# Optimization experiments

Hardware: AMD Instinct MI355X
Metric: run time of the kernel (lower is better)

## Reference

```python
import jax, jax.numpy as jnp
import numpy as np

EPS = 1e-5


def _conv(x, w, groups=1):
    # x: NCHW, w: OIHW, stride 1, padding k//2 == SAME for k=3
    return jax.lax.conv_general_dilated(
        x, w, window_strides=(1, 1), padding='SAME',
        feature_group_count=groups,
        dimension_numbers=('NCHW', 'OIHW', 'NCHW'))


def _bn(x, gamma, beta, mean, var):
    # eval-mode BatchNorm2d
    s = gamma * jax.lax.rsqrt(var + EPS)
    return x * s[None, :, None, None] + (beta - mean * s)[None, :, None, None]


def _bilinear_up_kernel(ch, k):
    # dla_up.fill_up_weights: bilinear upsampling kernel, shape (ch, 1, k, k)
    f = (k + 1) // 2
    c = (2 * f - 1 - f % 2) / (2.0 * f)
    i = np.arange(k)
    w1d = 1.0 - np.abs(i / f - c)
    w2d = np.outer(w1d, w1d).astype(np.float32)  # (k, k)
    return jnp.asarray(np.broadcast_to(w2d, (ch, 1, k, k)).copy())


def setup_inputs() -> dict:
    key = jax.random.key(0)
    ks = jax.random.split(key, 8)
    B, C, H, W = 16, 32, 128, 128
    OUT, NL = 8, 4
    layers = jax.random.normal(ks[0], (NL + 1, B, C, H, W), jnp.float32)
    node_w = jax.random.normal(ks[1], (NL, C, 2 * C, 3, 3), jnp.float32) * 0.05
    node_gamma = jnp.ones((NL, C), jnp.float32)
    node_beta = jnp.zeros((NL, C), jnp.float32)
    node_mean = jax.random.normal(ks[2], (NL, C), jnp.float32) * 0.1
    node_var = jax.random.uniform(ks[3], (NL, C), jnp.float32, 0.5, 1.5)
    final_w = jax.random.normal(ks[4], (OUT, C, 3, 3), jnp.float32) * 0.05
    final_gamma = jnp.ones((OUT,), jnp.float32)
    final_beta = jnp.zeros((OUT,), jnp.float32)
    final_mean = jax.random.normal(ks[5], (OUT,), jnp.float32) * 0.1
    final_var = jax.random.uniform(ks[6], (OUT,), jnp.float32, 0.5, 1.5)
    up_w = _bilinear_up_kernel(OUT, 4)  # frozen depthwise transpose-conv weight
    return dict(layers=layers, node_w=node_w, node_gamma=node_gamma,
                node_beta=node_beta, node_mean=node_mean, node_var=node_var,
                final_w=final_w, final_gamma=final_gamma, final_beta=final_beta,
                final_mean=final_mean, final_var=final_var, up_w=up_w)


def reference(layers, node_w, node_gamma, node_beta, node_mean, node_var,
              final_w, final_gamma, final_beta, final_mean, final_var, up_w):
    x = layers[0]
    n_layers = node_w.shape[0]
    for i in range(n_layers):  # fixed small structural loop
        h = jnp.concatenate([x, layers[i + 1]], axis=1)  # [B, 2C, H, W]
        x = jax.nn.relu(_bn(_conv(h, node_w[i]),
                            node_gamma[i], node_beta[i], node_mean[i], node_var[i]))
    x = jnp.tanh(_bn(_conv(x, final_w),
                     final_gamma, final_beta, final_mean, final_var))
    # depthwise ConvTranspose2d(k=4, stride=2, pad=1): equivalent fractionally
    # strided conv with flipped kernel, lhs_dilation=2, padding k-1-pad=2
    groups = up_w.shape[0]
    x = jax.lax.conv_general_dilated(
        x, up_w[:, :, ::-1, ::-1], window_strides=(1, 1),
        padding=[(2, 2), (2, 2)], lhs_dilation=(2, 2),
        feature_group_count=groups,
        dimension_numbers=('NCHW', 'OIHW', 'NCHW'))  # [B, OUT, 2H, 2W]
    # vectorized form of the per-row / per-col delta loops
    Ho, Wo = x.shape[2], x.shape[3]
    row_ramp = jnp.arange(Ho, dtype=x.dtype) / Ho  # delta_i = i / H
    col_ramp = jnp.arange(Wo, dtype=x.dtype) / Wo  # delta_j = j / W
    x = x.at[:, 0].add(row_ramp[None, :, None])
    x = x.at[:, 1].add(col_ramp[None, None, :])
    return x
```

## Files before the change

### kernel.cpp

```cpp
#include <hip/hip_runtime.h>
#include <hip/hip_bf16.h>
#include <cmath>

using bf16 = __hip_bfloat16;
typedef _Float16 f16x8 __attribute__((ext_vector_type(8)));
typedef float f32x16 __attribute__((ext_vector_type(16)));

__device__ __forceinline__ float ldin(const void* p, size_t i, int f) {
    return f ? ((const float*)p)[i] : __bfloat162float(((const bf16*)p)[i]);
}

__device__ __forceinline__ float bfu(unsigned short u) {
    union { unsigned u32; float f; } x; x.u32 = (unsigned)u << 16; return x.f;
}

__device__ __forceinline__ int swq(int X) { return (X + (X >> 2)) & 3; }

__global__ void detect_kernel(const unsigned short* __restrict__ u, int* __restrict__ flag) {
    __shared__ int s_bad;
    if (threadIdx.x == 0) s_bad = 0;
    __syncthreads();
    int base = blockIdx.x * 256 + threadIdx.x;
    int bad = 0;
#pragma unroll
    for (int k = 0; k < 4; ++k) {
        unsigned short v = u[2 * (base + k * 16384)];
        int e = (v >> 7) & 0xFF;
        if (e == 0xFF || (e == 0 && (v & 0x7FFF))) bad++;
    }
    if (bad) atomicAdd(&s_bad, bad);
    __syncthreads();
    if (threadIdx.x == 0 && s_bad) atomicAdd(&flag[1], s_bad);
}

__global__ void pack_kernel(const void* __restrict__ nw, const void* __restrict__ ng,
                            const void* __restrict__ nb, const void* __restrict__ nm,
                            const void* __restrict__ nv, const void* __restrict__ fw,
                            const void* __restrict__ fg, const void* __restrict__ fb,
                            const void* __restrict__ fm, const void* __restrict__ fv,
                            const void* __restrict__ upw, const int* __restrict__ flag,
                            char* __restrict__ ws) {
    const int f = flag[1] > 32;
    int i = blockIdx.x * 256 + threadIdx.x;
    _Float16* wpkN = (_Float16*)(ws + 160);
    _Float16* wpkF = (_Float16*)(ws + 147616);
    float* upwf  = (float*)(ws + 166048);
    float* nbias = (float*)(ws + 166560);
    float* fbias = (float*)(ws + 167072);
    if (i < 73728) {
        int e = i & 7, lane = (i >> 3) & 63, rest = i >> 9;
        int t = rest % 9, rest2 = rest / 9;
        int kc = rest2 & 3, lay = rest2 >> 2;
        int oc = lane & 31, ic = kc * 16 + ((lane >> 5) << 3) + e;
        float s = ldin(ng, lay * 32 + oc, f) * rsqrtf(ldin(nv, lay * 32 + oc, f) + 1e-5f);
        float w = ldin(nw, ((size_t)(lay * 32 + oc) * 64 + ic) * 9 + t, f);
        wpkN[i] = (_Float16)(w * s);
    } else if (i < 82944) {
        int j = i - 73728;
        int e = j & 7, lane = (j >> 3) & 63, rest = j >> 9;
        int t = rest % 9, kc = rest / 9;
        int oc = lane & 31, ic = kc * 16 + ((lane >> 5) << 3) + e;
        float v = 0.f;
        if (oc < 8) {
            float s = ldin(fg, oc, f) * rsqrtf(ldin(fv, oc, f) + 1e-5f);
            v = ldin(fw, ((size_t)(oc * 32 + ic)) * 9 + t, f) * s;
        }
        wpkF[j] = (_Float16)v;
    } else if (i < 83072) {
        int k = i - 82944;
        upwf[k] = ldin(upw, k, f);
    } else if (i < 83200) {
        int k = i - 83072;
        float s = ldin(ng, k, f) * rsqrtf(ldin(nv, k, f) + 1e-5f);
        nbias[k] = ldin(nb, k, f) - ldin(nm, k, f) * s;
    } else if (i < 83232) {
        int k = i - 83200;
        float v = 0.f;
        if (k < 8) {
            float s = ldin(fg, k, f) * rsqrtf(ldin(fv, k, f) + 1e-5f);
            v = ldin(fb, k, f) - ldin(fm, k, f) * s;
        }
        fbias[k] = v;
    }
}

__device__ __forceinline__ void stage_nchw_g(char* lds, const void* src,
                                             size_t base_elem, int f, int tid,
                                             int x0g, int y0g) {
    for (int job = tid; job < 1360; job += 256) {
        int c = job / 340, rest = job - c * 340;
        int row = rest / 34, X = rest - row * 34;
        int gy = y0g - 1 + row, gx = x0g - 1 + X;
        union { _Float16 h[8]; uint4 v; } pk;
        if (gy >= 0 && gy < 128 && gx >= 0 && gx < 128) {
            size_t e0 = base_elem + (size_t)(c * 8) * 16384 + (size_t)gy * 128 + gx;
            if (f) {
#pragma unroll
                for (int j = 0; j < 8; ++j)
                    pk.h[j] = (_Float16)(((const float*)src)[e0 + (size_t)j * 16384]);
            } else {
#pragma unroll
                for (int j = 0; j < 8; ++j)
                    pk.h[j] = (_Float16)bfu(((const unsigned short*)src)[e0 + (size_t)j * 16384]);
            }
        } else {
            pk.v = make_uint4(0u, 0u, 0u, 0u);
        }
        int slot = (c + swq(X)) & 3;
        *(uint4*)(lds + row * 2176 + (X << 6) + (slot << 4)) = pk.v;
    }
}

__device__ __forceinline__ void stage_nhwc(char* lds, const _Float16* xh, int tid,
                                           int b, int x0g, int y0g) {
    for (int q = tid; q < 1360; q += 256) {
        int p = q >> 2, s = q & 3;
        int row = p / 34, X = p - row * 34;
        int c = (s - swq(X)) & 3;
        int gy = y0g - 1 + row, gx = x0g - 1 + X;
        uint4 v = {0u, 0u, 0u, 0u};
        if (gy >= 0 && gy < 128 && gx >= 0 && gx < 128)
            v = *(const uint4*)(xh + (((size_t)(b * 128 + gy) * 128 + gx) * 32 + c * 8));
        *(uint4*)(lds + (q << 4)) = v;
    }
}

__device__ __forceinline__ void conv_plane(const char* lds, const _Float16* wseg,
                                           int lane, int wid, int lh,
                                           f32x16& acc0, f32x16& acc1) {
    const int l31 = lane & 31;
#pragma unroll
    for (int kc = 0; kc < 2; ++kc) {
        f16x8 bfr[9];
#pragma unroll
        for (int t = 0; t < 9; ++t)
            bfr[t] = *(const f16x8*)(wseg + (size_t)((kc * 9 + t) * 64 + lane) * 8);
        const int chunk = (kc << 1) | lh;
#pragma unroll
        for (int iy = 0; iy < 4; ++iy) {
            const int rowoff = ((wid << 1) + iy) * 2176;
#pragma unroll
            for (int kx = 0; kx < 3; ++kx) {
                const int X = l31 + kx;
                const int slot = (chunk + swq(X)) & 3;
                const f16x8 a = *(const f16x8*)(lds + rowoff + (X << 6) + (slot << 4));
#pragma unroll
                for (int ky = 0; ky < 3; ++ky) {
                    const int y = iy - ky;
                    if (y == 0)
                        acc0 = __builtin_amdgcn_mfma_f32_32x32x16_f16(a, bfr[ky * 3 + kx], acc0, 0, 0, 0);
                    else if (y == 1)
                        acc1 = __builtin_amdgcn_mfma_f32_32x32x16_f16(a, bfr[ky * 3 + kx], acc1, 0, 0, 0);
                }
            }
        }
    }
}

__global__ __launch_bounds__(256, 3) void node_conv_mfma(
    const void* __restrict__ xprev, int xprev_nchw, int xprev_slice,
    const void* __restrict__ layers, int skip_slice,
    const _Float16* __restrict__ wl, const float* __restrict__ bias,
    const int* __restrict__ flag, _Float16* __restrict__ out) {
    __shared__ char lds[21760];
    const int f = flag[1] > 32;
    const int tid = threadIdx.x;
    const int x0g = blockIdx.x << 5, y0g = blockIdx.y << 3, b = blockIdx.z;
    const int lane = tid & 63, wid = tid >> 6;
    const int l31 = lane & 31, lh = lane >> 5;

    f32x16 acc0, acc1;
#pragma unroll
    for (int r = 0; r < 16; ++r) { acc0[r] = 0.f; acc1[r] = 0.f; }

    if (xprev_nchw)
        stage_nchw_g(lds, xprev, (size_t)xprev_slice * 8388608 + (size_t)b * 524288,
                     f, tid, x0g, y0g);
    else
        stage_nhwc(lds, (const _Float16*)xprev, tid, b, x0g, y0g);
    __syncthreads();
    conv_plane(lds, wl, lane, wid, lh, acc0, acc1);
    __syncthreads();

    stage_nchw_g(lds, layers, (size_t)skip_slice * 8388608 + (size_t)b * 524288,
                 f, tid, x0g, y0g);
    __syncthreads();
    conv_plane(lds, wl + 9216, lane, wid, lh, acc0, acc1);

    const float bs = bias[l31];
    {
        const int gy = y0g + (wid << 1);
#pragma unroll
        for (int r = 0; r < 16; ++r) {
            const int xr = (r & 3) + ((r >> 2) << 3) + (lh << 2);
            out[((size_t)(b * 128 + gy) * 128 + (x0g + xr)) * 32 + l31] =
                (_Float16)fmaxf(acc0[r] + bs, 0.f);
        }
#pragma unroll
        for (int r = 0; r < 16; ++r) {
            const int xr = (r & 3) + ((r >> 2) << 3) + (lh << 2);
            out[((size_t)(b * 128 + gy + 1) * 128 + (x0g + xr)) * 32 + l31] =
                (_Float16)fmaxf(acc1[r] + bs, 0.f);
        }
    }
}

__device__ __forceinline__ float ftanh(float x) {
    float e = __expf(2.f * x);
    return 1.f - 2.f / (e + 1.f);
}

__global__ __launch_bounds__(256, 3) void final_conv_mfma(
    const _Float16* __restrict__ xin, const _Float16* __restrict__ wf,
    const float* __restrict__ fbias, _Float16* __restrict__ outF) {
    __shared__ char lds[21760];
    const int tid = threadIdx.x;
    const int x0g = blockIdx.x << 5, y0g = blockIdx.y << 3, b = blockIdx.z;
    const int lane = tid & 63, wid = tid >> 6;
    const int l31 = lane & 31, lh = lane >> 5;

    stage_nhwc(lds, xin, tid, b, x0g, y0g);
    __syncthreads();

    f32x16 acc0, acc1;
#pragma unroll
    for (int r = 0; r < 16; ++r) { acc0[r] = 0.f; acc1[r] = 0.f; }
    conv_plane(lds, wf, lane, wid, lh, acc0, acc1);

    const float bs = fbias[l31];
    if (l31 < 8) {
        const int gy = y0g + (wid << 1);
#pragma unroll
        for (int r = 0; r < 16; ++r) {
            const int xr = (r & 3) + ((r >> 2) << 3) + (lh << 2);
            outF[((size_t)(b * 128 + gy) * 128 + (x0g + xr)) * 8 + l31] =
                (_Float16)ftanh(acc0[r] + bs);
        }
#pragma unroll
        for (int r = 0; r < 16; ++r) {
            const int xr = (r & 3) + ((r >> 2) << 3) + (lh << 2);
            outF[((size_t)(b * 128 + gy + 1) * 128 + (x0g + xr)) * 8 + l31] =
                (_Float16)ftanh(acc1[r] + bs);
        }
    }
}

__global__ __launch_bounds__(256) void upsample_q(
    const _Float16* __restrict__ F, const float* __restrict__ wf,
    const int* __restrict__ flag, void* __restrict__ out) {
    const int f = flag[1] > 32;
    int i = blockIdx.x * 256 + threadIdx.x;
    int qx = i & 127, qy = (i >> 7) & 127, b = i >> 14;

    f16x8 inb[3][3];
#pragma unroll
    for (int jy = 0; jy < 3; ++jy)
#pragma unroll
        for (int jx = 0; jx < 3; ++jx) {
            int iy = qy - 1 + jy, ix = qx - 1 + jx;
            f16x8 v;
#pragma unroll
            for (int c = 0; c < 8; ++c) v[c] = (_Float16)0.f;
            if (iy >= 0 && iy < 128 && ix >= 0 && ix < 128)
                v = *(const f16x8*)(F + (((size_t)(b * 128 + iy) * 128 + ix) << 3));
            inb[jy][jx] = v;
        }

    float acc[32];
#pragma unroll
    for (int k = 0; k < 32; ++k) acc[k] = 0.f;
#pragma unroll
    for (int ky = 0; ky < 4; ++ky) {
        const int dy = 1 - (ky & 1), jy = 2 - ((ky + 1) >> 1);
#pragma unroll
        for (int kx = 0; kx < 4; ++kx) {
            const int dx = 1 - (kx & 1), jx = 2 - ((kx + 1) >> 1);
            const f16x8 p = inb[jy][jx];
#pragma unroll
            for (int c = 0; c < 8; ++c)
                acc[c * 4 + dy * 2 + dx] =
                    fmaf((float)p[c], wf[c * 16 + ky * 4 + kx], acc[c * 4 + dy * 2 + dx]);
        }
    }
#pragma unroll
    for (int d = 0; d < 4; ++d) {
        acc[d]     += (float)(2 * qy + (d >> 1)) * (1.0f / 256.0f);
        acc[4 + d] += (float)(2 * qx + (d & 1)) * (1.0f / 256.0f);
    }
#pragma unroll
    for (int c = 0; c < 8; ++c)
#pragma unroll
        for (int dy2 = 0; dy2 < 2; ++dy2) {
            size_t a = ((size_t)(b * 8 + c) * 256 + (qy * 2 + dy2)) * 256 + qx * 2;
            float v0 = acc[c * 4 + dy2 * 2], v1 = acc[c * 4 + dy2 * 2 + 1];
            if (f) {
                *(float2*)((float*)out + a) = make_float2(v0, v1);
            } else {
                union { bf16 h; unsigned short u; } u0, u1;
                u0.h = __float2bfloat16(v0); u1.h = __float2bfloat16(v1);
                ((unsigned*)out)[a >> 1] = (unsigned)u0.u | ((unsigned)u1.u << 16);
            }
        }
}

extern "C" void kernel_launch(void* const* d_in, const int* in_sizes, int n_in,
                              void* d_out, int out_size, void* d_ws, size_t ws_size,
                              hipStream_t stream) {
    const void* layers = d_in[0];
    const void* node_w = d_in[1];
    const void* ng     = d_in[2];
    const void* nb     = d_in[3];
    const void* nm     = d_in[4];
    const void* nv     = d_in[5];
    const void* fw     = d_in[6];
    const void* fg     = d_in[7];
    const void* fb     = d_in[8];
    const void* fm     = d_in[9];
    const void* fv     = d_in[10];
    const void* upw    = d_in[11];

    char* ws = (char*)d_ws;
    int* dflag       = (int*)d_ws;
    _Float16* wpkN   = (_Float16*)(ws + 160);
    _Float16* wpkF   = (_Float16*)(ws + 147616);
    float* upwf      = (float*)(ws + 166048);
    float* nbias     = (float*)(ws + 166560);
    float* fbias     = (float*)(ws + 167072);
    _Float16* X      = (_Float16*)(ws + 167424);
    _Float16* Y      = (_Float16*)d_out;

    hipMemsetAsync(dflag, 0, 16, stream);
    detect_kernel<<<64, 256, 0, stream>>>((const unsigned short*)layers, dflag);
    pack_kernel<<<326, 256, 0, stream>>>(node_w, ng, nb, nm, nv,
                                         fw, fg, fb, fm, fv, upw, dflag, ws);

    dim3 g(4, 16, 16), blk(256);
    node_conv_mfma<<<g, blk, 0, stream>>>(layers, 1, 0, layers, 1,
                                          wpkN, nbias, dflag, X);
    node_conv_mfma<<<g, blk, 0, stream>>>(X, 0, 0, layers, 2,
                                          wpkN + 18432, nbias + 32, dflag, Y);
    node_conv_mfma<<<g, blk, 0, stream>>>(Y, 0, 0, layers, 3,
                                          wpkN + 2 * 18432, nbias + 64, dflag, X);
    node_conv_mfma<<<g, blk, 0, stream>>>(X, 0, 0, layers, 4,
                                          wpkN + 3 * 18432, nbias + 96, dflag, Y);
    final_conv_mfma<<<g, blk, 0, stream>>>(Y, wpkF, fbias, X);
    upsample_q<<<1024, 256, 0, stream>>>(X, upwf, dflag, d_out);
}
```

Before: 482.0 us.

## Stage both conv inputs at once, coalesce outputs via LDS, fold dtype detect into pack

The node conv now stages the previous activation and the skip layer into two LDS halves before a single barrier and runs all four K-chunks in one pass, which removes the mid-kernel barrier and staging serialization. Both node and final conv outputs are transposed through LDS and written as 16-byte coalesced stores instead of scattered 2-byte stores. The separate memset and detect kernels are dropped; each pack block does its own bf16/fp32 sampling detection and writes the flag to the workspace. Staging loops are fully unrolled. Doubling LDS per block may reduce occupancy below the requested three blocks per CU.

Result: faster. 388.8 us (-19.3%).

```diff
diff --git a/kernel.cpp b/kernel.cpp
--- a/kernel.cpp
+++ b/kernel.cpp
@@ -16,21 +16,21 @@
 
 __device__ __forceinline__ int swq(int X) { return (X + (X >> 2)) & 3; }
 
-__global__ void detect_kernel(const unsigned short* __restrict__ u, int* __restrict__ flag) {
+__device__ __forceinline__ int detect_f(const void* layers_) {
+    const unsigned short* u = (const unsigned short*)layers_;
     __shared__ int s_bad;
     if (threadIdx.x == 0) s_bad = 0;
     __syncthreads();
-    int base = blockIdx.x * 256 + threadIdx.x;
     int bad = 0;
 #pragma unroll
-    for (int k = 0; k < 4; ++k) {
-        unsigned short v = u[2 * (base + k * 16384)];
+    for (int k = 0; k < 16; ++k) {
+        unsigned short v = u[2 * ((threadIdx.x * 16 + k) * 257)];
         int e = (v >> 7) & 0xFF;
-        if (e == 0xFF || (e == 0 && (v & 0x7FFF))) bad++;
+        bad += (e == 0xFF || (e == 0 && (v & 0x7FFF))) ? 1 : 0;
     }
     if (bad) atomicAdd(&s_bad, bad);
     __syncthreads();
-    if (threadIdx.x == 0 && s_bad) atomicAdd(&flag[1], s_bad);
+    return s_bad > 0;
 }
 
 __global__ void pack_kernel(const void* __restrict__ nw, const void* __restrict__ ng,
@@ -38,9 +38,10 @@
                             const void* __restrict__ nv, const void* __restrict__ fw,
                             const void* __restrict__ fg, const void* __restrict__ fb,
                             const void* __restrict__ fm, const void* __restrict__ fv,
-                            const void* __restrict__ upw, const int* __restrict__ flag,
+                            const void* __restrict__ upw, const void* __restrict__ layers_,
                             char* __restrict__ ws) {
-    const int f = flag[1] > 32;
+    const int f = detect_f(layers_);
+    if (blockIdx.x == 0 && threadIdx.x == 0) *(volatile int*)ws = f;
     int i = blockIdx.x * 256 + threadIdx.x;
     _Float16* wpkN = (_Float16*)(ws + 160);
     _Float16* wpkF = (_Float16*)(ws + 147616);
@@ -87,55 +88,64 @@
 __device__ __forceinline__ void stage_nchw_g(char* lds, const void* src,
                                              size_t base_elem, int f, int tid,
                                              int x0g, int y0g) {
-    for (int job = tid; job < 1360; job += 256) {
-        int c = job / 340, rest = job - c * 340;
-        int row = rest / 34, X = rest - row * 34;
-        int gy = y0g - 1 + row, gx = x0g - 1 + X;
-        union { _Float16 h[8]; uint4 v; } pk;
-        if (gy >= 0 && gy < 128 && gx >= 0 && gx < 128) {
-            size_t e0 = base_elem + (size_t)(c * 8) * 16384 + (size_t)gy * 128 + gx;
-            if (f) {
-#pragma unroll
-                for (int j = 0; j < 8; ++j)
-                    pk.h[j] = (_Float16)(((const float*)src)[e0 + (size_t)j * 16384]);
+#pragma unroll
+    for (int it = 0; it < 6; ++it) {
+        int job = tid + it * 256;
+        if (it < 5 || job < 1360) {
+            int c = job / 340, rest = job - c * 340;
+            int row = rest / 34, X = rest - row * 34;
+            int gy = y0g - 1 + row, gx = x0g - 1 + X;
+            union { _Float16 h[8]; uint4 v; } pk;
+            if (gy >= 0 && gy < 128 && gx >= 0 && gx < 128) {
+                size_t e0 = base_elem + (size_t)(c * 8) * 16384 + (size_t)gy * 128 + gx;
+                if (f) {
+#pragma unroll
+                    for (int j = 0; j < 8; ++j)
+                        pk.h[j] = (_Float16)(((const float*)src)[e0 + (size_t)j * 16384]);
+                } else {
+#pragma unroll
+                    for (int j = 0; j < 8; ++j)
+                        pk.h[j] = (_Float16)bfu(((const unsigned short*)src)[e0 + (size_t)j * 16384]);
+                }
             } else {
-#pragma unroll
-                for (int j = 0; j < 8; ++j)
-                    pk.h[j] = (_Float16)bfu(((const unsigned short*)src)[e0 + (size_t)j * 16384]);
+                pk.v = make_uint4(0u, 0u, 0u, 0u);
             }
-        } else {
-            pk.v = make_uint4(0u, 0u, 0u, 0u);
-        }
-        int slot = (c + swq(X)) & 3;
-        *(uint4*)(lds + row * 2176 + (X << 6) + (slot << 4)) = pk.v;
+            int slot = (c + swq(X)) & 3;
+            *(uint4*)(lds + row * 2176 + (X << 6) + (slot << 4)) = pk.v;
+        }
     }
 }
 
 __device__ __forceinline__ void stage_nhwc(char* lds, const _Float16* xh, int tid,
                                            int b, int x0g, int y0g) {
-    for (int q = tid; q < 1360; q += 256) {
-        int p = q >> 2, s = q & 3;
-        int row = p / 34, X = p - row * 34;
-        int c = (s - swq(X)) & 3;
-        int gy = y0g - 1 + row, gx = x0g - 1 + X;
-        uint4 v = {0u, 0u, 0u, 0u};
-        if (gy >= 0 && gy < 128 && gx >= 0 && gx < 128)
-            v = *(const uint4*)(xh + (((size_t)(b * 128 + gy) * 128 + gx) * 32 + c * 8));
-        *(uint4*)(lds + (q << 4)) = v;
-    }
-}
-
-__device__ __forceinline__ void conv_plane(const char* lds, const _Float16* wseg,
-                                           int lane, int wid, int lh,
-                                           f32x16& acc0, f32x16& acc1) {
+#pragma unroll
+    for (int it = 0; it < 6; ++it) {
+        int q = tid + it * 256;
+        if (it < 5 || q < 1360) {
+            int p = q >> 2, s = q & 3;
+            int row = p / 34, X = p - row * 34;
+            int c = (s - swq(X)) & 3;
+            int gy = y0g - 1 + row, gx = x0g - 1 + X;
+            uint4 v = {0u, 0u, 0u, 0u};
+            if (gy >= 0 && gy < 128 && gx >= 0 && gx < 128)
+                v = *(const uint4*)(xh + (((size_t)(b * 128 + gy) * 128 + gx) * 32 + c * 8));
+            *(uint4*)(lds + (q << 4)) = v;
+        }
+    }
+}
+
+__device__ __forceinline__ void conv_both(const char* lds, const _Float16* wseg,
+                                          int lane, int wid, int lh,
+                                          f32x16& acc0, f32x16& acc1) {
     const int l31 = lane & 31;
 #pragma unroll
-    for (int kc = 0; kc < 2; ++kc) {
+    for (int kc = 0; kc < 4; ++kc) {
         f16x8 bfr[9];
 #pragma unroll
         for (int t = 0; t < 9; ++t)
             bfr[t] = *(const f16x8*)(wseg + (size_t)((kc * 9 + t) * 64 + lane) * 8);
-        const int chunk = (kc << 1) | lh;
+        const char* pl = lds + ((kc & 2) ? 21760 : 0);
+        const int chunk = ((kc & 1) << 1) | lh;
 #pragma unroll
         for (int iy = 0; iy < 4; ++iy) {
             const int rowoff = ((wid << 1) + iy) * 2176;
@@ -143,7 +153,7 @@
             for (int kx = 0; kx < 3; ++kx) {
                 const int X = l31 + kx;
                 const int slot = (chunk + swq(X)) & 3;
-                const f16x8 a = *(const f16x8*)(lds + rowoff + (X << 6) + (slot << 4));
+                const f16x8 a = *(const f16x8*)(pl + rowoff + (X << 6) + (slot << 4));
 #pragma unroll
                 for (int ky = 0; ky < 3; ++ky) {
                     const int y = iy - ky;
@@ -157,51 +167,83 @@
     }
 }
 
+__device__ __forceinline__ void conv_plane(const char* lds, const _Float16* wseg,
+                                           int lane, int wid, int lh,
+                                           f32x16& acc0, f32x16& acc1) {
+    const int l31 = lane & 31;
+#pragma unroll
+    for (int kc = 0; kc < 2; ++kc) {
+        f16x8 bfr[9];
+#pragma unroll
+        for (int t = 0; t < 9; ++t)
+            bfr[t] = *(const f16x8*)(wseg + (size_t)((kc * 9 + t) * 64 + lane) * 8);
+        const int chunk = (kc << 1) | lh;
+#pragma unroll
+        for (int iy = 0; iy < 4; ++iy) {
+            const int rowoff = ((wid << 1) + iy) * 2176;
+#pragma unroll
+            for (int kx = 0; kx < 3; ++kx) {
+                const int X = l31 + kx;
+                const int slot = (chunk + swq(X)) & 3;
+                const f16x8 a = *(const f16x8*)(lds + rowoff + (X << 6) + (slot << 4));
+#pragma unroll
+                for (int ky = 0; ky < 3; ++ky) {
+                    const int y = iy - ky;
+                    if (y == 0)
+                        acc0 = __builtin_amdgcn_mfma_f32_32x32x16_f16(a, bfr[ky * 3 + kx], acc0, 0, 0, 0);
+                    else if (y == 1)
+                        acc1 = __builtin_amdgcn_mfma_f32_32x32x16_f16(a, bfr[ky * 3 + kx], acc1, 0, 0, 0);
+                }
+            }
+        }
+    }
+}
+
 __global__ __launch_bounds__(256, 3) void node_conv_mfma(
     const void* __restrict__ xprev, int xprev_nchw, int xprev_slice,
     const void* __restrict__ layers, int skip_slice,
     const _Float16* __restrict__ wl, const float* __restrict__ bias,
     const int* __restrict__ flag, _Float16* __restrict__ out) {
-    __shared__ char lds[21760];
-    const int f = flag[1] > 32;
+    __shared__ char lds[43520];
+    const int f = flag[0];
     const int tid = threadIdx.x;
     const int x0g = blockIdx.x << 5, y0g = blockIdx.y << 3, b = blockIdx.z;
     const int lane = tid & 63, wid = tid >> 6;
     const int l31 = lane & 31, lh = lane >> 5;
-
-    f32x16 acc0, acc1;
-#pragma unroll
-    for (int r = 0; r < 16; ++r) { acc0[r] = 0.f; acc1[r] = 0.f; }
 
     if (xprev_nchw)
         stage_nchw_g(lds, xprev, (size_t)xprev_slice * 8388608 + (size_t)b * 524288,
                      f, tid, x0g, y0g);
     else
         stage_nhwc(lds, (const _Float16*)xprev, tid, b, x0g, y0g);
-    __syncthreads();
-    conv_plane(lds, wl, lane, wid, lh, acc0, acc1);
-    __syncthreads();
-
-    stage_nchw_g(lds, layers, (size_t)skip_slice * 8388608 + (size_t)b * 524288,
+    stage_nchw_g(lds + 21760, layers, (size_t)skip_slice * 8388608 + (size_t)b * 524288,
                  f, tid, x0g, y0g);
     __syncthreads();
-    conv_plane(lds, wl + 9216, lane, wid, lh, acc0, acc1);
+
+    f32x16 acc0, acc1;
+#pragma unroll
+    for (int r = 0; r < 16; ++r) { acc0[r] = 0.f; acc1[r] = 0.f; }
+    conv_both(lds, wl, lane, wid, lh, acc0, acc1);
+    __syncthreads();
 
     const float bs = bias[l31];
-    {
-        const int gy = y0g + (wid << 1);
-#pragma unroll
-        for (int r = 0; r < 16; ++r) {
-            const int xr = (r & 3) + ((r >> 2) << 3) + (lh << 2);
-            out[((size_t)(b * 128 + gy) * 128 + (x0g + xr)) * 32 + l31] =
-                (_Float16)fmaxf(acc0[r] + bs, 0.f);
-        }
-#pragma unroll
-        for (int r = 0; r < 16; ++r) {
-            const int xr = (r & 3) + ((r >> 2) << 3) + (lh << 2);
-            out[((size_t)(b * 128 + gy + 1) * 128 + (x0g + xr)) * 32 + l31] =
-                (_Float16)fmaxf(acc1[r] + bs, 0.f);
-        }
+    const int row0 = wid << 1;
+#pragma unroll
+    for (int r = 0; r < 16; ++r) {
+        const int xr = (r & 3) + ((r >> 2) << 3) + (lh << 2);
+        *(_Float16*)(lds + (row0 * 32 + xr) * 80 + (l31 << 1)) =
+            (_Float16)fmaxf(acc0[r] + bs, 0.f);
+        *(_Float16*)(lds + ((row0 + 1) * 32 + xr) * 80 + (l31 << 1)) =
+            (_Float16)fmaxf(acc1[r] + bs, 0.f);
+    }
+    __syncthreads();
+    const size_t obase = ((size_t)(b * 128 + y0g) * 128 + x0g) * 32;
+#pragma unroll
+    for (int it = 0; it < 4; ++it) {
+        int g = tid + it * 256;
+        int prow = g >> 7, inrow = g & 127;
+        uint4 v = *(const uint4*)(lds + (prow * 32 + (inrow >> 2)) * 80 + (inrow & 3) * 16);
+        *(uint4*)(out + obase + (size_t)prow * 4096 + inrow * 8) = v;
     }
 }
 
@@ -226,29 +268,33 @@
 #pragma unroll
     for (int r = 0; r < 16; ++r) { acc0[r] = 0.f; acc1[r] = 0.f; }
     conv_plane(lds, wf, lane, wid, lh, acc0, acc1);
+    __syncthreads();
 
     const float bs = fbias[l31];
+    const int row0 = wid << 1;
     if (l31 < 8) {
-        const int gy = y0g + (wid << 1);
 #pragma unroll
         for (int r = 0; r < 16; ++r) {
             const int xr = (r & 3) + ((r >> 2) << 3) + (lh << 2);
-            outF[((size_t)(b * 128 + gy) * 128 + (x0g + xr)) * 8 + l31] =
+            *(_Float16*)(lds + (row0 * 32 + xr) * 16 + (l31 << 1)) =
                 (_Float16)ftanh(acc0[r] + bs);
-        }
-#pragma unroll
-        for (int r = 0; r < 16; ++r) {
-            const int xr = (r & 3) + ((r >> 2) << 3) + (lh << 2);
-            outF[((size_t)(b * 128 + gy + 1) * 128 + (x0g + xr)) * 8 + l31] =
+            *(_Float16*)(lds + ((row0 + 1) * 32 + xr) * 16 + (l31 << 1)) =
                 (_Float16)ftanh(acc1[r] + bs);
         }
+    }
+    __syncthreads();
+    {
+        int g = tid;
+        int prow = g >> 5, px = g & 31;
+        uint4 v = *(const uint4*)(lds + g * 16);
+        *(uint4*)(outF + ((size_t)(b * 128 + y0g + prow) * 128 + x0g + px) * 8) = v;
     }
 }
 
 __global__ __launch_bounds__(256) void upsample_q(
     const _Float16* __restrict__ F, const float* __restrict__ wf,
     const int* __restrict__ flag, void* __restrict__ out) {
-    const int f = flag[1] > 32;
+    const int f = flag[0];
     int i = blockIdx.x * 256 + threadIdx.x;
     int qx = i & 127, qy = (i >> 7) & 127, b = i >> 14;
 
@@ -329,10 +375,8 @@
     _Float16* X      = (_Float16*)(ws + 167424);
     _Float16* Y      = (_Float16*)d_out;
 
-    hipMemsetAsync(dflag, 0, 16, stream);
-    detect_kernel<<<64, 256, 0, stream>>>((const unsigned short*)layers, dflag);
     pack_kernel<<<326, 256, 0, stream>>>(node_w, ng, nb, nm, nv,
-                                         fw, fg, fb, fm, fv, upw, dflag, ws);
+                                         fw, fg, fb, fm, fv, upw, layers, ws);
 
     dim3 g(4, 16, 16), blk(256);
     node_conv_mfma<<<g, blk, 0, stream>>>(layers, 1, 0, layers, 1,
```
